# Optimization experiments

Hardware: AMD Instinct MI355X
Metric: run time of the kernel (lower is better)

The kernel has to match this reference:

```python
import jax, jax.numpy as jnp
import numpy as np

N_ROW = 512
N_COL = 512
N_RAY = 131072   # ~256 views x 512 detector channels
N_INT = 768      # padded max grid-line intersections per ray


def setup_inputs() -> dict:
    key = jax.random.key(0)
    k1, k2, k3, k4 = jax.random.split(key, 4)
    image = jax.random.normal(k1, (N_ROW, N_COL), dtype=jnp.float32)
    # sorted ray parameters in [0, 1] (fractions along src->dst)
    t_sorted = jnp.sort(jax.random.uniform(k2, (N_RAY, N_INT), dtype=jnp.float32), axis=-1)
    M = jnp.eye(2, dtype=jnp.float32)          # pixel spacing = 1
    b = jnp.zeros((2,), dtype=jnp.float32)     # image origin at (0, 0)
    # fan-beam-like geometry: sources on a circle around image center
    center = jnp.array([255.5, 255.5], dtype=jnp.float32)
    radius = 400.0
    ang = jax.random.uniform(k3, (N_RAY,), dtype=jnp.float32, minval=0.0, maxval=2.0 * np.pi)
    off = jax.random.uniform(k4, (N_RAY,), dtype=jnp.float32, minval=-0.3, maxval=0.3)
    src = center + radius * jnp.stack([jnp.cos(ang), jnp.sin(ang)], axis=-1)
    dst = center - radius * jnp.stack([jnp.cos(ang + off), jnp.sin(ang + off)], axis=-1)
    return {"image": image, "t_sorted": t_sorted, "M": M, "b": b, "src": src, "dst": dst}


def reference(image, t_sorted, M, b, src, dst):
    n_row, n_col = image.shape
    M_inv = jnp.linalg.inv(M)
    # intersection points along each ray: [n_ray, n_int, 2]
    pts = src[:, None, :] + t_sorted[:, :, None] * (dst - src)[:, None, :]
    x0, y0 = pts[:, :-1, 0], pts[:, :-1, 1]
    x1, y1 = pts[:, 1:, 0], pts[:, 1:, 1]
    inf_mask = jnp.isinf(x0) | jnp.isinf(x1) | jnp.isinf(y0) | jnp.isinf(y1)
    seg_len = jnp.sqrt((x1 - x0) ** 2 + (y1 - y0) ** 2)
    # segment midpoints -> pixel indices via inverse affine transform
    mx = 0.5 * (x0 + x1) - b[0]
    my = 0.5 * (y0 + y1) - b[1]
    rowf = M_inv[0, 0] * mx + M_inv[0, 1] * my
    colf = M_inv[1, 0] * mx + M_inv[1, 1] * my
    row_idx = jnp.round(rowf).astype(jnp.int32)
    col_idx = jnp.round(colf).astype(jnp.int32)
    oob = (row_idx < 0) | (row_idx >= n_row) | (col_idx < 0) | (col_idx >= n_col)
    valid = (~inf_mask) & (~oob)
    flat_idx = jnp.where(valid, row_idx * n_col + col_idx, 0)
    pixel_vals = image.reshape(-1)[flat_idx]          # gather [n_ray, n_int-1]
    segment_val = jnp.where(valid, pixel_vals * seg_len, 0.0)
    return segment_val.sum(axis=1)                    # sinogram [n_ray]
```

## Files before the change

kernel.cpp:

```cpp
#include <hip/hip_runtime.h>

#define N_ROW 512
#define N_COL 512
#define N_INT 768
#define N_SEG (N_INT - 1)
#define WPB 4

__global__ __launch_bounds__(WPB * 64)
void ct_fwd_kernel(const float* __restrict__ image,
                   const float* __restrict__ t_sorted,
                   const float* __restrict__ M,
                   const float* __restrict__ b,
                   const float* __restrict__ src,
                   const float* __restrict__ dst,
                   float* __restrict__ out,
                   int n_ray)
{
#pragma clang fp contract(off)
    const int wave = threadIdx.x >> 6;
    const int lane = threadIdx.x & 63;
    const int ray  = blockIdx.x * WPB + wave;
    if (ray >= n_ray) return;

    const float m00 = M[0], m01 = M[1], m10 = M[2], m11 = M[3];
    const float det  = m00 * m11 - m01 * m10;
    const float rdet = 1.0f / det;
    const float i00 =  m11 * rdet;
    const float i01 = -(m01 * rdet);
    const float i10 = -(m10 * rdet);
    const float i11 =  m00 * rdet;
    const float b0 = b[0], b1 = b[1];

    const float sx  = src[2 * ray];
    const float sy  = src[2 * ray + 1];
    const float ddx = dst[2 * ray]     - sx;
    const float ddy = dst[2 * ray + 1] - sy;

    const float* __restrict__ tp = t_sorted + (size_t)ray * N_INT;

    float tv[12];
#pragma unroll
    for (int c = 0; c < 12; ++c)
        tv[c] = tp[c * 64 + lane];

    float tu[12];
#pragma unroll
    for (int c = 0; c < 12; ++c) {
        float u = __shfl_down(tv[c], 1, 64);
        if (c < 11) {
            const float brd = __shfl(tv[c + 1], 0, 64);
            if (lane == 63) u = brd;
        }
        tu[c] = u;
    }

    float acc = 0.0f;
#pragma unroll
    for (int c = 0; c < 12; ++c) {
        const float t0 = tv[c];
        const float t1 = tu[c];

        const float px0 = t0 * ddx;
        const float py0 = t0 * ddy;
        const float px1 = t1 * ddx;
        const float py1 = t1 * ddy;
        const float x0 = sx + px0;
        const float y0 = sy + py0;
        const float x1 = sx + px1;
        const float y1 = sy + py1;

        const float ex = x1 - x0;
        const float ey = y1 - y0;
        const float ex2 = ex * ex;
        const float ey2 = ey * ey;
        const float seg = __fsqrt_rn(ex2 + ey2);

        const float sxm = x0 + x1;
        const float sym = y0 + y1;
        const float mx = 0.5f * sxm - b0;
        const float my = 0.5f * sym - b1;

        const float r0 = i00 * mx;
        const float r1 = i01 * my;
        const float c0 = i10 * mx;
        const float c1 = i11 * my;
        const float rowf = r0 + r1;
        const float colf = c0 + c1;

        const int ri = (int)rintf(rowf);
        const int ci = (int)rintf(colf);

        const bool segv = !((c == 11) & (lane == 63));
        const bool valid = (ri >= 0) & (ri < N_ROW) &
                           (ci >= 0) & (ci < N_COL) & segv;
        const int flat = valid ? (ri * N_COL + ci) : 0;
        const float pv = image[flat];
        acc += valid ? pv * seg : 0.0f;
    }

#pragma unroll
    for (int off = 32; off > 0; off >>= 1)
        acc += __shfl_down(acc, off, 64);

    if (lane == 0) out[ray] = acc;
}

extern "C" void kernel_launch(void* const* d_in, const int* in_sizes, int n_in,
                              void* d_out, int out_size, void* d_ws, size_t ws_size,
                              hipStream_t stream)
{
    const float* image    = (const float*)d_in[0];
    const float* t_sorted = (const float*)d_in[1];
    const float* M        = (const float*)d_in[2];
    const float* b        = (const float*)d_in[3];
    const float* src      = (const float*)d_in[4];
    const float* dst      = (const float*)d_in[5];
    float* out = (float*)d_out;

    const int n_ray = in_sizes[4] / 2;
    const int grid = (n_ray + WPB - 1) / WPB;
    ct_fwd_kernel<<<grid, WPB * 64, 0, stream>>>(
        image, t_sorted, M, b, src, dst, out, n_ray);
}
```

Measured before the change: 625.7 us.

## Retile image into 4x4 blocks for gather locality and stream t via nontemporal loads

Adds a pre-pass that copies the image into a 4x4-blocked layout in the workspace, and the main kernel indexes that layout so gathers from lanes at nearby pixels fall in the same cache lines. Loads of t_sorted, src and dst and the output store become nontemporal so the large streaming input is less likely to evict the image from cache. The cost is an extra kernel launch and a 1 MB copy on every call, plus a fallback path used when the workspace is too small.

```diff
diff --git a/kernel.cpp b/kernel.cpp
--- a/kernel.cpp
+++ b/kernel.cpp
@@ -5,7 +5,22 @@
 #define N_INT 768
 #define N_SEG (N_INT - 1)
 #define WPB 4
+#define IMG_ELEMS (N_ROW * N_COL)
 
+__global__ __launch_bounds__(256)
+void tile_image_kernel(const float* __restrict__ img, float* __restrict__ img_t)
+{
+    const int idx    = blockIdx.x * 256 + threadIdx.x;
+    const int within = idx & 15;
+    const int tile   = idx >> 4;
+    const int tc = tile & 127;
+    const int tr = tile >> 7;
+    const int ri = (tr << 2) | (within >> 2);
+    const int ci = (tc << 2) | (within & 3);
+    img_t[idx] = img[ri * N_COL + ci];
+}
+
+template<bool TILED>
 __global__ __launch_bounds__(WPB * 64)
 void ct_fwd_kernel(const float* __restrict__ image,
                    const float* __restrict__ t_sorted,
@@ -31,17 +46,17 @@
     const float i11 =  m00 * rdet;
     const float b0 = b[0], b1 = b[1];
 
-    const float sx  = src[2 * ray];
-    const float sy  = src[2 * ray + 1];
-    const float ddx = dst[2 * ray]     - sx;
-    const float ddy = dst[2 * ray + 1] - sy;
+    const float sx  = __builtin_nontemporal_load(&src[2 * ray]);
+    const float sy  = __builtin_nontemporal_load(&src[2 * ray + 1]);
+    const float ddx = __builtin_nontemporal_load(&dst[2 * ray])     - sx;
+    const float ddy = __builtin_nontemporal_load(&dst[2 * ray + 1]) - sy;
 
     const float* __restrict__ tp = t_sorted + (size_t)ray * N_INT;
 
     float tv[12];
 #pragma unroll
     for (int c = 0; c < 12; ++c)
-        tv[c] = tp[c * 64 + lane];
+        tv[c] = __builtin_nontemporal_load(&tp[c * 64 + lane]);
 
     float tu[12];
 #pragma unroll
@@ -93,7 +108,15 @@
         const bool segv = !((c == 11) & (lane == 63));
         const bool valid = (ri >= 0) & (ri < N_ROW) &
                            (ci >= 0) & (ci < N_COL) & segv;
-        const int flat = valid ? (ri * N_COL + ci) : 0;
+
+        int flat;
+        if (TILED) {
+            flat = valid ? (((ri >> 2) << 11) | ((ci >> 2) << 4) |
+                            ((ri & 3) << 2)  | (ci & 3))
+                         : 0;
+        } else {
+            flat = valid ? (ri * N_COL + ci) : 0;
+        }
         const float pv = image[flat];
         acc += valid ? pv * seg : 0.0f;
     }
@@ -102,7 +125,7 @@
     for (int off = 32; off > 0; off >>= 1)
         acc += __shfl_down(acc, off, 64);
 
-    if (lane == 0) out[ray] = acc;
+    if (lane == 0) __builtin_nontemporal_store(acc, &out[ray]);
 }
 
 extern "C" void kernel_launch(void* const* d_in, const int* in_sizes, int n_in,
@@ -119,6 +142,14 @@
 
     const int n_ray = in_sizes[4] / 2;
     const int grid = (n_ray + WPB - 1) / WPB;
-    ct_fwd_kernel<<<grid, WPB * 64, 0, stream>>>(
-        image, t_sorted, M, b, src, dst, out, n_ray);
+
+    if (ws_size >= (size_t)IMG_ELEMS * sizeof(float)) {
+        float* img_t = (float*)d_ws;
+        tile_image_kernel<<<IMG_ELEMS / 256, 256, 0, stream>>>(image, img_t);
+        ct_fwd_kernel<true><<<grid, WPB * 64, 0, stream>>>(
+            img_t, t_sorted, M, b, src, dst, out, n_ray);
+    } else {
+        ct_fwd_kernel<false><<<grid, WPB * 64, 0, stream>>>(
+            image, t_sorted, M, b, src, dst, out, n_ray);
+    }
 }
```

Result: faster. 589.0 us (-5.9%).
